# Kernel optimization log

Hardware: AMD Instinct MI355X
Metric: run time of the kernel (lower is better)

Reference implementation:

```python
import jax, jax.numpy as jnp
import numpy as np
import math

H = 128  # hidden_dim
RADIUS = 30.0


def _lin(x, w, b):
    return x @ w + b


def _masked_softmax(logits, mask):
    return jax.nn.softmax(jnp.where(mask, logits, -1e9), axis=-1)


def setup_inputs() -> dict:
    key = jax.random.key(0)
    ks = iter(jax.random.split(key, 64))

    def p(shape, s=0.02):
        return (jax.random.normal(next(ks), shape, jnp.float32) * s)

    B, N, T, M, L = 2, 48, 24, 192, 20
    inp = {
        'agents_state': jax.random.normal(next(ks), (B, N, T, 5), jnp.float32),
        'agents_mask': jnp.ones((B, N, T), jnp.float32),
        'map_polylines': jax.random.normal(next(ks), (B, M, L, 2), jnp.float32),
        'map_poly_mask': jnp.ones((B, M), jnp.float32),
        'map_poly_type': jax.random.randint(next(ks), (B, M), 0, 4),
        'map_tl_status': jax.random.randint(next(ks), (B, M), 0, 8),
        'map_on_route': jax.random.randint(next(ks), (B, M), 0, 2),
        # AgentStateEncoder
        'ae_w0': p((5, H)), 'ae_b0': p((H,)), 'ae_w1': p((H, H)), 'ae_b1': p((H,)),
        'ae_w2': p((H, H)), 'ae_b2': p((H,)),
        # MapPolylineNodeEncoder point_mlp
        'mp_w0': p((2, H)), 'mp_b0': p((H,)), 'mp_w1': p((H, H)), 'mp_b1': p((H,)),
        'type_emb': p((4, H)), 'tl_emb': p((8, H)), 'route_emb': p((2, H)),
        'mo_w0': p((H, H)), 'mo_b0': p((H,)), 'mo_w1': p((H, H)), 'mo_b1': p((H,)),
        # map_rel_mlp (3 -> H -> 1)
        'mr_w0': p((3, H)), 'mr_b0': p((H,)), 'mr_w1': p((H, 1)), 'mr_b1': p((1,)),
        # nbr_rel_mlp (5 -> H -> 1)
        'nr_w0': p((5, H)), 'nr_b0': p((H,)), 'nr_w1': p((H, 1)), 'nr_b1': p((1,)),
        # tau_out (3H -> H -> 64)
        'to_w0': p((3 * H, H)), 'to_b0': p((H,)), 'to_w1': p((H, 64)), 'to_b1': p((64,)),
    }
    return inp


def reference(agents_state, agents_mask, map_polylines, map_poly_mask,
              map_poly_type, map_tl_status, map_on_route,
              ae_w0, ae_b0, ae_w1, ae_b1, ae_w2, ae_b2,
              mp_w0, mp_b0, mp_w1, mp_b1, type_emb, tl_emb, route_emb,
              mo_w0, mo_b0, mo_w1, mo_b1,
              mr_w0, mr_b0, mr_w1, mr_b1,
              nr_w0, nr_b0, nr_w1, nr_b1,
              to_w0, to_b0, to_w1, to_b1):
    B, N, T, _ = agents_state.shape
    a_mask = agents_mask > 0.5
    a_feat = agents_state[..., :5]

    # --- MapPolylineNodeEncoder ---
    m = map_poly_mask > 0.5
    h = jax.nn.relu(_lin(jax.nn.relu(_lin(map_polylines, mp_w0, mp_b0)), mp_w1, mp_b1))  # B,M,L,H
    h = h.max(axis=2)  # B,M,H
    pt = jnp.clip(map_poly_type, 0, type_emb.shape[0] - 1)
    tl = jnp.clip(map_tl_status, 0, tl_emb.shape[0] - 1)
    rt = jnp.clip(map_on_route, 0, route_emb.shape[0] - 1)
    h = h + type_emb[pt] + tl_emb[tl] + route_emb[rt]
    h = _lin(jax.nn.relu(_lin(h, mo_w0, mo_b0)), mo_w1, mo_b1)
    map_node = h * m[..., None].astype(h.dtype)  # B,M,D
    map_center = map_polylines.mean(axis=2)  # B,M,2

    # --- AgentStateEncoder ---
    a = jax.nn.relu(_lin(a_feat, ae_w0, ae_b0))
    a = jax.nn.relu(_lin(a, ae_w1, ae_b1))
    a_emb = _lin(a, ae_w2, ae_b2) * a_mask[..., None].astype(a.dtype)  # B,N,T,D

    # --- map cross-attention with relative-position bias ---
    agent_pos = a_feat[..., 0:2]
    rel = map_center[:, None, None, :, :] - agent_pos[:, :, :, None, :]  # B,N,T,M,2
    dist = jnp.linalg.norm(rel, axis=-1, keepdims=True)
    rel_feat = jnp.concatenate([rel, dist], axis=-1)  # B,N,T,M,3
    rel_score = _lin(jax.nn.relu(_lin(rel_feat, mr_w0, mr_b0)), mr_w1, mr_b1)[..., 0]  # B,N,T,M
    dot = jnp.einsum('bntd,bmd->bntm', a_emb, map_node) / math.sqrt(map_node.shape[-1])
    attn = _masked_softmax(dot + rel_score, m[:, None, None, :])
    map_ctx = jnp.einsum('bntm,bmd->bntd', attn, map_node)

    # --- neighbor graph attention ---
    pos = a_feat[..., 0:2]
    vel = a_feat[..., 3:5]
    rel_pos = jnp.transpose(pos[:, :, None] - pos[:, None, :], (0, 1, 3, 2, 4))  # B,N,T,N,2
    rel_vel = jnp.transpose(vel[:, :, None] - vel[:, None, :], (0, 1, 3, 2, 4))
    dist_ij = jnp.linalg.norm(rel_pos, axis=-1, keepdims=True)  # B,N,T,N,1
    rel_ij = jnp.concatenate([rel_pos, rel_vel, dist_ij], axis=-1)  # B,N,T,N,5
    nbr_score = _lin(jax.nn.relu(_lin(rel_ij, nr_w0, nr_b0)), nr_w1, nr_b1)[..., 0]  # B,N,T,N

    valid_i = a_mask[..., None]  # B,N,T,1
    valid_j = jnp.transpose(a_mask, (0, 2, 1))[:, None, :, :]  # B,1,T,N
    radius_ok = dist_ij[..., 0] <= RADIUS
    not_self = ~jnp.eye(N, dtype=bool)[None, :, None, :]  # 1,N,1,N
    nbr_mask = valid_i & valid_j & radius_ok & not_self

    dot_n = jnp.einsum('bntd,bjtd->bntj', a_emb, a_emb) / math.sqrt(a_emb.shape[-1])
    w_n = _masked_softmax(dot_n + nbr_score, nbr_mask)  # B,N,T,N
    nbr_ctx = jnp.einsum('bntj,bjtd->bntd', w_n, a_emb)

    tau = jnp.concatenate([a_emb, map_ctx, nbr_ctx], axis=-1)
    tau = _lin(jax.nn.relu(_lin(tau, to_w0, to_b0)), to_w1, to_b1)
    tau = tau * a_mask[..., None].astype(tau.dtype)
    return tau, map_ctx, nbr_ctx
```

## Files before the change

### kernel.cpp

```cpp
#include <hip/hip_runtime.h>
#include <math.h>

#define HH 128
#define BB 2
#define NN 48
#define TT 24
#define MM 192
#define LL 20
#define NT (BB*NN*TT)
#define RSQRT_H 0.08838834764831845f
#define RADIUS_C 30.0f

__global__ __launch_bounds__(512) void k_map_enc(
    const float* __restrict__ polylines, const float* __restrict__ poly_mask,
    const int* __restrict__ ptype, const int* __restrict__ tlst, const int* __restrict__ route,
    const float* __restrict__ mp_w0, const float* __restrict__ mp_b0,
    const float* __restrict__ mp_w1, const float* __restrict__ mp_b1,
    const float* __restrict__ type_emb, const float* __restrict__ tl_emb,
    const float* __restrict__ route_emb,
    const float* __restrict__ mo_w0, const float* __restrict__ mo_b0,
    const float* __restrict__ mo_w1, const float* __restrict__ mo_b1,
    float* __restrict__ map_node, float* __restrict__ map_nodeT,
    float* __restrict__ map_center)
{
    int bm  = blockIdx.x;
    int tid = threadIdx.x;
    int pp  = tid >> 7;
    int c   = tid & 127;

    __shared__ float pts[LL*2];
    __shared__ float h1[LL][HH];
    __shared__ float mx[4][HH];
    __shared__ float hb[HH];
    __shared__ float pr[4][HH];
    __shared__ float hb2[HH];

    if (tid < LL*2) pts[tid] = polylines[(size_t)bm*LL*2 + tid];
    __syncthreads();

    {
        float w0x = mp_w0[c], w0y = mp_w0[HH + c], b0 = mp_b0[c];
        #pragma unroll
        for (int i = 0; i < 5; ++i) {
            int p = pp + 4*i;
            h1[p][c] = fmaxf(fmaf(pts[2*p], w0x, fmaf(pts[2*p+1], w0y, b0)), 0.f);
        }
    }
    if (tid < 2) {
        float s = 0.f;
        for (int p = 0; p < LL; ++p) s += pts[2*p + tid];
        map_center[bm*2 + tid] = s * (1.0f / LL);
    }
    __syncthreads();

    {
        float acc[5];
        float b1 = mp_b1[c];
        #pragma unroll
        for (int i = 0; i < 5; ++i) acc[i] = b1;
        for (int k = 0; k < HH; ++k) {
            float wv = mp_w1[k*HH + c];
            #pragma unroll
            for (int i = 0; i < 5; ++i) acc[i] = fmaf(h1[pp + 4*i][k], wv, acc[i]);
        }
        float m5 = acc[0];
        #pragma unroll
        for (int i = 1; i < 5; ++i) m5 = fmaxf(m5, acc[i]);
        mx[pp][c] = m5;
    }
    __syncthreads();

    if (tid < HH) {
        float hm = fmaxf(fmaxf(mx[0][c], mx[1][c]), fmaxf(mx[2][c], mx[3][c]));
        hm = fmaxf(hm, 0.f);
        int pt = ptype[bm]; pt = pt < 0 ? 0 : (pt > 3 ? 3 : pt);
        int tv = tlst[bm];  tv = tv < 0 ? 0 : (tv > 7 ? 7 : tv);
        int rv = route[bm]; rv = rv < 0 ? 0 : (rv > 1 ? 1 : rv);
        hm += type_emb[pt*HH + c] + tl_emb[tv*HH + c] + route_emb[rv*HH + c];
        hb[c] = hm;
    }
    __syncthreads();

    {
        float s = 0.f;
        int k0 = pp*32;
        for (int k = k0; k < k0 + 32; ++k) s = fmaf(hb[k], mo_w0[k*HH + c], s);
        pr[pp][c] = s;
    }
    __syncthreads();
    if (tid < HH) hb2[c] = fmaxf(pr[0][c] + pr[1][c] + pr[2][c] + pr[3][c] + mo_b0[c], 0.f);
    __syncthreads();
    {
        float s = 0.f;
        int k0 = pp*32;
        for (int k = k0; k < k0 + 32; ++k) s = fmaf(hb2[k], mo_w1[k*HH + c], s);
        pr[pp][c] = s;
    }
    __syncthreads();
    if (tid < HH) {
        float a3 = pr[0][c] + pr[1][c] + pr[2][c] + pr[3][c] + mo_b1[0*HH + c];
        float mk = (poly_mask[bm] > 0.5f) ? 1.f : 0.f;
        float v = a3 * mk;
        map_node[(size_t)bm*HH + c] = v;
        int b = bm / MM, m = bm % MM;
        map_nodeT[((size_t)b*HH + c)*MM + m] = v;
    }
}

__global__ __launch_bounds__(256) void k_agent_enc(
    const float* __restrict__ astate, const float* __restrict__ amask,
    const float* __restrict__ ae_w0, const float* __restrict__ ae_b0,
    const float* __restrict__ ae_w1, const float* __restrict__ ae_b1,
    const float* __restrict__ ae_w2, const float* __restrict__ ae_b2,
    float* __restrict__ a_emb)
{
    int r0  = blockIdx.x * 4;
    int tid = threadIdx.x;
    int h   = tid >> 7;
    int c   = tid & 127;

    __shared__ float xin[4][5];
    __shared__ float h1[4][HH];
    __shared__ float h2[4][HH];
    __shared__ float p1[2][4][HH];

    if (tid < 20) xin[tid/5][tid%5] = astate[(size_t)r0*5 + tid];
    __syncthreads();

    if (h == 0) {
        float b = ae_b0[c];
        float w[5];
        #pragma unroll
        for (int i = 0; i < 5; ++i) w[i] = ae_w0[i*HH + c];
        #pragma unroll
        for (int r = 0; r < 4; ++r) {
            float v = b;
            #pragma unroll
            for (int i = 0; i < 5; ++i) v = fmaf(xin[r][i], w[i], v);
            h1[r][c] = fmaxf(v, 0.f);
        }
    }
    __syncthreads();

    {
        float acc[4] = {0.f, 0.f, 0.f, 0.f};
        int k0 = h*64;
        for (int k = k0; k < k0 + 64; ++k) {
            float wv = ae_w1[k*HH + c];
            #pragma unroll
            for (int r = 0; r < 4; ++r) acc[r] = fmaf(h1[r][k], wv, acc[r]);
        }
        #pragma unroll
        for (int r = 0; r < 4; ++r) p1[h][r][c] = acc[r];
    }
    __syncthreads();
    {
        #pragma unroll
        for (int rr = 0; rr < 2; ++rr) {
            int r = h*2 + rr;
            h2[r][c] = fmaxf(p1[0][r][c] + p1[1][r][c] + ae_b1[c], 0.f);
        }
    }
    __syncthreads();

    {
        float acc[4] = {0.f, 0.f, 0.f, 0.f};
        int k0 = h*64;
        for (int k = k0; k < k0 + 64; ++k) {
            float wv = ae_w2[k*HH + c];
            #pragma unroll
            for (int r = 0; r < 4; ++r) acc[r] = fmaf(h2[r][k], wv, acc[r]);
        }
        #pragma unroll
        for (int r = 0; r < 4; ++r) p1[h][r][c] = acc[r];
    }
    __syncthreads();
    {
        #pragma unroll
        for (int rr = 0; rr < 2; ++rr) {
            int r = h*2 + rr;
            int row = r0 + r;
            float v = (p1[0][r][c] + p1[1][r][c] + ae_b2[c]) * amask[row];
            a_emb[(size_t)row*HH + c] = v;
        }
    }
}

__global__ __launch_bounds__(256) void k_map_attn(
    const float* __restrict__ astate,
    const float* __restrict__ a_emb, const float* __restrict__ map_node,
    const float* __restrict__ map_nodeT, const float* __restrict__ map_center,
    const float* __restrict__ poly_mask,
    const float* __restrict__ mr_w0, const float* __restrict__ mr_b0,
    const float* __restrict__ mr_w1, const float* __restrict__ mr_b1,
    float* __restrict__ map_ctx)
{
    int bnt0 = blockIdx.x * 4;
    int b    = bnt0 / (NN*TT);
    int tid  = threadIdx.x;

    __shared__ float  mnL[16][MM];
    __shared__ float4 w4L[HH];
    __shared__ float  w1L[HH];
    __shared__ float4 aq4L[HH];
    __shared__ float  lg[4][MM];
    __shared__ float4 p4L[MM];
    __shared__ float  invL[4];
    __shared__ float  pc[2][4][HH];

    if (tid < HH) {
        int k = tid;
        w4L[k] = make_float4(mr_w0[k], mr_w0[HH+k], mr_w0[2*HH+k], mr_b0[k]);
        w1L[k] = mr_w1[k];
    }
    for (int idx = tid; idx < 4*HH; idx += 256) {
        int r = idx >> 7, k = idx & 127;
        ((float*)&aq4L[k])[r] = a_emb[(size_t)(bnt0 + r)*HH + k];
    }

    float rx[4], ry[4], rd[4];
    if (tid < MM) {
        float mcx = map_center[(b*MM + tid)*2];
        float mcy = map_center[(b*MM + tid)*2 + 1];
        #pragma unroll
        for (int r = 0; r < 4; ++r) {
            float px = astate[(size_t)(bnt0 + r)*5];
            float py = astate[(size_t)(bnt0 + r)*5 + 1];
            rx[r] = mcx - px; ry[r] = mcy - py;
            rd[r] = sqrtf(rx[r]*rx[r] + ry[r]*ry[r]);
        }
    }

    const float* mnT = map_nodeT + (size_t)b*HH*MM;
    float4 st[3];
    #pragma unroll
    for (int i = 0; i < 3; ++i) {
        int q = tid + 256*i;
        int kk = q / 48, mq = q % 48;
        st[i] = *(const float4*)(mnT + (size_t)kk*MM + mq*4);
    }
    float s[4]  = {0.f,0.f,0.f,0.f};
    float dt[4] = {0.f,0.f,0.f,0.f};
    for (int ch = 0; ch < 8; ++ch) {
        __syncthreads();
        #pragma unroll
        for (int i = 0; i < 3; ++i) {
            int q = tid + 256*i;
            int kk = q / 48, mq = q % 48;
            *(float4*)&mnL[kk][mq*4] = st[i];
        }
        __syncthreads();
        if (ch < 7) {
            #pragma unroll
            for (int i = 0; i < 3; ++i) {
                int q = tid + 256*i;
                int kk = q / 48, mq = q % 48;
                st[i] = *(const float4*)(mnT + (size_t)(ch+1)*16*MM + (size_t)kk*MM + mq*4);
            }
        }
        if (tid < MM) {
            int k0 = ch*16;
            #pragma unroll
            for (int kk = 0; kk < 16; ++kk) {
                int k = k0 + kk;
                float4 w  = w4L[k];
                float  w1 = w1L[k];
                float4 aq = aq4L[k];
                float  mn = mnL[kk][tid];
                #pragma unroll
                for (int r = 0; r < 4; ++r) {
                    float hv = fmaf(rx[r], w.x, fmaf(ry[r], w.y, fmaf(rd[r], w.z, w.w)));
                    s[r] = fmaf(fmaxf(hv, 0.f), w1, s[r]);
                }
                dt[0] = fmaf(aq.x, mn, dt[0]);
                dt[1] = fmaf(aq.y, mn, dt[1]);
                dt[2] = fmaf(aq.z, mn, dt[2]);
                dt[3] = fmaf(aq.w, mn, dt[3]);
            }
        }
    }

    if (tid < MM) {
        float pm = poly_mask[b*MM + tid];
        float b1 = mr_b1[0];
        #pragma unroll
        for (int r = 0; r < 4; ++r) {
            float lgt = fmaf(dt[r], RSQRT_H, s[r] + b1);
            lg[r][tid] = (pm > 0.5f) ? lgt : -1e9f;
        }
    }
    __syncthreads();

    {
        int r = tid >> 6, l = tid & 63;
        float v = fmaxf(fmaxf(lg[r][l], lg[r][l+64]), lg[r][l+128]);
        #pragma unroll
        for (int o = 32; o > 0; o >>= 1) v = fmaxf(v, __shfl_xor(v, o));
        float e0 = expf(lg[r][l] - v);
        float e1 = expf(lg[r][l+64] - v);
        float e2 = expf(lg[r][l+128] - v);
        lg[r][l] = e0; lg[r][l+64] = e1; lg[r][l+128] = e2;
        float sm = e0 + e1 + e2;
        #pragma unroll
        for (int o = 32; o > 0; o >>= 1) sm += __shfl_xor(sm, o);
        if (l == 0) invL[r] = 1.0f / sm;
    }
    __syncthreads();
    if (tid < MM) {
        p4L[tid] = make_float4(lg[0][tid]*invL[0], lg[1][tid]*invL[1],
                               lg[2][tid]*invL[2], lg[3][tid]*invL[3]);
    }
    __syncthreads();

    {
        int half = tid >> 7, c = tid & 127;
        float a0=0.f, a1=0.f, a2=0.f, a3=0.f;
        const float* mnb = map_node + ((size_t)b*MM + half*96)*HH + c;
        for (int m = 0; m < 96; ++m) {
            float mv = mnb[(size_t)m*HH];
            float4 p = p4L[half*96 + m];
            a0 = fmaf(p.x, mv, a0); a1 = fmaf(p.y, mv, a1);
            a2 = fmaf(p.z, mv, a2); a3 = fmaf(p.w, mv, a3);
        }
        pc[half][0][c]=a0; pc[half][1][c]=a1; pc[half][2][c]=a2; pc[half][3][c]=a3;
    }
    __syncthreads();
    for (int idx = tid; idx < 4*HH; idx += 256) {
        int r = idx >> 7, c = idx & 127;
        map_ctx[(size_t)(bnt0 + r)*HH + c] = pc[0][r][c] + pc[1][r][c];
    }
}

__global__ __launch_bounds__(256) void k_nbr_attn(
    const float* __restrict__ astate, const float* __restrict__ amask,
    const float* __restrict__ a_emb,
    const float* __restrict__ nr_w0, const float* __restrict__ nr_b0,
    const float* __restrict__ nr_w1, const float* __restrict__ nr_b1,
    float* __restrict__ nbr_ctx)
{
    int bid = blockIdx.x;
    int b   = bid / (TT*8);
    int rem = bid % (TT*8);
    int t   = rem / 8;
    int n0  = (rem % 8) * 6;
    int tid = threadIdx.x;

    __shared__ float  aVL[NN][129];
    __shared__ float  pjL[NN][8];
    __shared__ float4 wAL[HH], wBL[HH];
    __shared__ float  aqL[HH][8];
    __shared__ float  sPL[4][6][NN], dPL[4][6][NN];
    __shared__ float  lgL[6][NN];
    __shared__ float  pL[NN][8];
    __shared__ float  pcL[2][6][HH];

    if (tid < NN) {
        int rj = (b*NN + tid)*TT + t;
        pjL[tid][0] = astate[(size_t)rj*5];
        pjL[tid][1] = astate[(size_t)rj*5 + 1];
        pjL[tid][2] = astate[(size_t)rj*5 + 3];
        pjL[tid][3] = astate[(size_t)rj*5 + 4];
        pjL[tid][4] = amask[rj];
    }
    if (tid < HH) {
        int k = tid;
        wAL[k] = make_float4(nr_w0[k], nr_w0[HH+k], nr_w0[2*HH+k], nr_w0[3*HH+k]);
        wBL[k] = make_float4(nr_w0[4*HH+k], nr_b0[k], nr_w1[k], 0.f);
    }
    #pragma unroll
    for (int i = 0; i < 6; ++i) {
        int q = tid + 256*i;
        int j = q >> 5, cq = q & 31;
        float4 v = *(const float4*)(a_emb + ((size_t)(b*NN + j)*TT + t)*HH + cq*4);
        aVL[j][cq*4+0] = v.x; aVL[j][cq*4+1] = v.y;
        aVL[j][cq*4+2] = v.z; aVL[j][cq*4+3] = v.w;
    }
    __syncthreads();
    for (int idx = tid; idx < 6*HH; idx += 256) {
        int r = idx >> 7, k = idx & 127;
        aqL[k][r] = aVL[n0 + r][k];
    }
    __syncthreads();

    int j  = tid % 48;
    int kg = tid / 48;
    float s[6]  = {0,0,0,0,0,0};
    float dt[6] = {0,0,0,0,0,0};
    if (kg < 4) {
        float jx = pjL[j][0], jy = pjL[j][1], jvx = pjL[j][2], jvy = pjL[j][3];
        float dx[6], dy[6], dvx[6], dvy[6], dd[6];
        #pragma unroll
        for (int r = 0; r < 6; ++r) {
            dx[r]  = pjL[n0+r][0] - jx;  dy[r]  = pjL[n0+r][1] - jy;
            dvx[r] = pjL[n0+r][2] - jvx; dvy[r] = pjL[n0+r][3] - jvy;
            dd[r]  = sqrtf(dx[r]*dx[r] + dy[r]*dy[r]);
        }
        int k0 = kg*32;
        for (int kk = 0; kk < 32; ++kk) {
            int k = k0 + kk;
            float4 wa = wAL[k], wb = wBL[k];
            float4 aA = *(const float4*)&aqL[k][0];
            float4 aB = *(const float4*)&aqL[k][4];
            float  av = aVL[j][k];
            #pragma unroll
            for (int r = 0; r < 6; ++r) {
                float hv = fmaf(dx[r], wa.x, fmaf(dy[r], wa.y,
                           fmaf(dvx[r], wa.z, fmaf(dvy[r], wa.w,
                           fmaf(dd[r], wb.x, wb.y)))));
                s[r] = fmaf(fmaxf(hv, 0.f), wb.z, s[r]);
            }
            dt[0] = fmaf(aA.x, av, dt[0]); dt[1] = fmaf(aA.y, av, dt[1]);
            dt[2] = fmaf(aA.z, av, dt[2]); dt[3] = fmaf(aA.w, av, dt[3]);
            dt[4] = fmaf(aB.x, av, dt[4]); dt[5] = fmaf(aB.y, av, dt[5]);
        }
        #pragma unroll
        for (int r = 0; r < 6; ++r) { sPL[kg][r][j] = s[r]; dPL[kg][r][j] = dt[r]; }
    }
    __syncthreads();

    float b1 = nr_b1[0];
    for (int idx = tid; idx < 6*NN; idx += 256) {
        int r = idx / NN, jj = idx % NN;
        int ni = n0 + r;
        float ss = sPL[0][r][jj] + sPL[1][r][jj] + sPL[2][r][jj] + sPL[3][r][jj] + b1;
        float do2 = dPL[0][r][jj] + dPL[1][r][jj] + dPL[2][r][jj] + dPL[3][r][jj];
        float ddx = pjL[ni][0] - pjL[jj][0];
        float ddy = pjL[ni][1] - pjL[jj][1];
        float dist = sqrtf(ddx*ddx + ddy*ddy);
        bool ok = (pjL[ni][4] > 0.5f) && (pjL[jj][4] > 0.5f) &&
                  (dist <= RADIUS_C) && (jj != ni);
        lgL[r][jj] = ok ? fmaf(do2, RSQRT_H, ss) : -1e9f;
    }
    __syncthreads();

    {
        int wv = tid >> 6, l = tid & 63;
        for (int r = wv; r < 6; r += 4) {
            float v = (l < NN) ? lgL[r][l] : -3.4e38f;
            #pragma unroll
            for (int o = 32; o > 0; o >>= 1) v = fmaxf(v, __shfl_xor(v, o));
            float e = (l < NN) ? expf(lgL[r][l] - v) : 0.f;
            float sm = e;
            #pragma unroll
            for (int o = 32; o > 0; o >>= 1) sm += __shfl_xor(sm, o);
            if (l < NN) lgL[r][l] = e / sm;
        }
    }
    __syncthreads();
    if (tid < NN) {
        #pragma unroll
        for (int r = 0; r < 6; ++r) pL[tid][r] = lgL[r][tid];
        pL[tid][6] = 0.f; pL[tid][7] = 0.f;
    }
    __syncthreads();

    {
        int half = tid >> 7, c = tid & 127;
        float acc[6] = {0,0,0,0,0,0};
        for (int jj = half*24; jj < half*24 + 24; ++jj) {
            float av = aVL[jj][c];
            float4 pA = *(const float4*)&pL[jj][0];
            float4 pB = *(const float4*)&pL[jj][4];
            acc[0] = fmaf(pA.x, av, acc[0]); acc[1] = fmaf(pA.y, av, acc[1]);
            acc[2] = fmaf(pA.z, av, acc[2]); acc[3] = fmaf(pA.w, av, acc[3]);
            acc[4] = fmaf(pB.x, av, acc[4]); acc[5] = fmaf(pB.y, av, acc[5]);
        }
        #pragma unroll
        for (int r = 0; r < 6; ++r) pcL[half][r][c] = acc[r];
    }
    __syncthreads();
    for (int idx = tid; idx < 6*HH; idx += 256) {
        int r = idx >> 7, c = idx & 127;
        int row = (b*NN + n0 + r)*TT + t;
        nbr_ctx[(size_t)row*HH + c] = pcL[0][r][c] + pcL[1][r][c];
    }
}

__global__ __launch_bounds__(512) void k_tau(
    const float* __restrict__ amask,
    const float* __restrict__ a_emb, const float* __restrict__ map_ctx,
    const float* __restrict__ nbr_ctx,
    const float* __restrict__ to_w0, const float* __restrict__ to_b0,
    const float* __restrict__ to_w1, const float* __restrict__ to_b1,
    float* __restrict__ tau)
{
    int r0  = blockIdx.x * 8;
    int tid = threadIdx.x;
    __shared__ float xinT[3*HH][8];
    __shared__ float p1L[4][8][HH];
    __shared__ float h1T[HH][8];
    __shared__ float p2L[8][8][64];

    #pragma unroll
    for (int i = 0; i < 2; ++i) {
        int q = tid + 512*i;
        if (q < 768) {
            int r = q / 96, kq = q % 96;
            const float* src;
            int co;
            if (kq < 32)      { src = a_emb;   co = kq; }
            else if (kq < 64) { src = map_ctx; co = kq - 32; }
            else              { src = nbr_ctx; co = kq - 64; }
            float4 v = *(const float4*)(src + (size_t)(r0 + r)*HH + co*4);
            int kbase = (kq < 32 ? 0 : (kq < 64 ? HH : 2*HH)) + co*4;
            xinT[kbase+0][r] = v.x; xinT[kbase+1][r] = v.y;
            xinT[kbase+2][r] = v.z; xinT[kbase+3][r] = v.w;
        }
    }
    __syncthreads();
    {
        int c = tid & 127, h = tid >> 7;
        float acc[8] = {0,0,0,0,0,0,0,0};
        for (int k = h*96; k < h*96 + 96; ++k) {
            float wv = to_w0[k*HH + c];
            float4 xa = *(const float4*)&xinT[k][0];
            float4 xb = *(const float4*)&xinT[k][4];
            acc[0]=fmaf(xa.x,wv,acc[0]); acc[1]=fmaf(xa.y,wv,acc[1]);
            acc[2]=fmaf(xa.z,wv,acc[2]); acc[3]=fmaf(xa.w,wv,acc[3]);
            acc[4]=fmaf(xb.x,wv,acc[4]); acc[5]=fmaf(xb.y,wv,acc[5]);
            acc[6]=fmaf(xb.z,wv,acc[6]); acc[7]=fmaf(xb.w,wv,acc[7]);
        }
        #pragma unroll
        for (int r = 0; r < 8; ++r) p1L[h][r][c] = acc[r];
    }
    __syncthreads();
    for (int idx = tid; idx < 8*HH; idx += 512) {
        int r = idx >> 7, k = idx & 127;
        float v = p1L[0][r][k] + p1L[1][r][k] + p1L[2][r][k] + p1L[3][r][k] + to_b0[k];
        h1T[k][r] = fmaxf(v, 0.f);
    }
    __syncthreads();
    {
        int c2 = tid & 63, h2 = tid >> 6;
        float acc[8] = {0,0,0,0,0,0,0,0};
        for (int k = h2*16; k < h2*16 + 16; ++k) {
            float wv = to_w1[k*64 + c2];
            float4 xa = *(const float4*)&h1T[k][0];
            float4 xb = *(const float4*)&h1T[k][4];
            acc[0]=fmaf(xa.x,wv,acc[0]); acc[1]=fmaf(xa.y,wv,acc[1]);
            acc[2]=fmaf(xa.z,wv,acc[2]); acc[3]=fmaf(xa.w,wv,acc[3]);
            acc[4]=fmaf(xb.x,wv,acc[4]); acc[5]=fmaf(xb.y,wv,acc[5]);
            acc[6]=fmaf(xb.z,wv,acc[6]); acc[7]=fmaf(xb.w,wv,acc[7]);
        }
        #pragma unroll
        for (int r = 0; r < 8; ++r) p2L[h2][r][c2] = acc[r];
    }
    __syncthreads();
    {
        int r = tid >> 6, c2 = tid & 63;
        float v = 0.f;
        #pragma unroll
        for (int h2 = 0; h2 < 8; ++h2) v += p2L[h2][r][c2];
        v = (v + to_b1[c2]) * amask[r0 + r];
        tau[(size_t)(r0 + r)*64 + c2] = v;
    }
}

extern "C" void kernel_launch(void* const* d_in, const int* in_sizes, int n_in,
                              void* d_out, int out_size, void* d_ws, size_t ws_size,
                              hipStream_t stream)
{
    const float* astate    = (const float*)d_in[0];
    const float* amask     = (const float*)d_in[1];
    const float* polylines = (const float*)d_in[2];
    const float* poly_mask = (const float*)d_in[3];
    const int*   ptype     = (const int*)d_in[4];
    const int*   tlst      = (const int*)d_in[5];
    const int*   route     = (const int*)d_in[6];
    const float* ae_w0 = (const float*)d_in[7];
    const float* ae_b0 = (const float*)d_in[8];
    const float* ae_w1 = (const float*)d_in[9];
    const float* ae_b1 = (const float*)d_in[10];
    const float* ae_w2 = (const float*)d_in[11];
    const float* ae_b2 = (const float*)d_in[12];
    const float* mp_w0 = (const float*)d_in[13];
    const float* mp_b0 = (const float*)d_in[14];
    const float* mp_w1 = (const float*)d_in[15];
    const float* mp_b1 = (const float*)d_in[16];
    const float* type_emb  = (const float*)d_in[17];
    const float* tl_emb    = (const float*)d_in[18];
    const float* route_emb = (const float*)d_in[19];
    const float* mo_w0 = (const float*)d_in[20];
    const float* mo_b0 = (const float*)d_in[21];
    const float* mo_w1 = (const float*)d_in[22];
    const float* mo_b1 = (const float*)d_in[23];
    const float* mr_w0 = (const float*)d_in[24];
    const float* mr_b0 = (const float*)d_in[25];
    const float* mr_w1 = (const float*)d_in[26];
    const float* mr_b1 = (const float*)d_in[27];
    const float* nr_w0 = (const float*)d_in[28];
    const float* nr_b0 = (const float*)d_in[29];
    const float* nr_w1 = (const float*)d_in[30];
    const float* nr_b1 = (const float*)d_in[31];
    const float* to_w0 = (const float*)d_in[32];
    const float* to_b0 = (const float*)d_in[33];
    const float* to_w1 = (const float*)d_in[34];
    const float* to_b1 = (const float*)d_in[35];

    float* tau     = (float*)d_out;
    float* map_ctx = (float*)d_out + (size_t)NT*64;
    float* nbr_ctx = map_ctx + (size_t)NT*HH;

    float* ws         = (float*)d_ws;
    float* a_emb      = ws;
    float* map_node   = a_emb + (size_t)NT*HH;
    float* map_nodeT  = map_node + (size_t)BB*MM*HH;
    float* map_center = map_nodeT + (size_t)BB*MM*HH;

    k_map_enc<<<BB*MM, 512, 0, stream>>>(polylines, poly_mask, ptype, tlst, route,
        mp_w0, mp_b0, mp_w1, mp_b1, type_emb, tl_emb, route_emb,
        mo_w0, mo_b0, mo_w1, mo_b1, map_node, map_nodeT, map_center);

    k_agent_enc<<<NT/4, 256, 0, stream>>>(astate, amask,
        ae_w0, ae_b0, ae_w1, ae_b1, ae_w2, ae_b2, a_emb);

    k_map_attn<<<NT/4, 256, 0, stream>>>(astate, a_emb, map_node, map_nodeT,
        map_center, poly_mask, mr_w0, mr_b0, mr_w1, mr_b1, map_ctx);

    k_nbr_attn<<<BB*TT*8, 256, 0, stream>>>(astate, amask, a_emb,
        nr_w0, nr_b0, nr_w1, nr_b1, nbr_ctx);

    k_tau<<<NT/8, 512, 0, stream>>>(amask, a_emb, map_ctx, nbr_ctx,
        to_w0, to_b0, to_w1, to_b1, tau);
}
```

Measured before the change: 202.7 us.

## Fuse all stages into one persistent kernel with grid barriers

Replaces the five separate kernel launches with a single persistent kernel of 512 blocks that loops over tasks and uses atomic-counter grid barriers between the encoder, attention and output stages. Shared memory is a union of per-stage structs, and each stage is reworked to run with 256 threads (map encoder and tau now use 2-way instead of 4/8-way k splits). The aim is to remove launch overhead and tail gaps between the small stages. In exchange it needs all 512 blocks co-resident for the spin barrier to avoid deadlock, adds a memset, and gives less parallelism per task in some stages.

```diff
diff --git a/kernel.cpp b/kernel.cpp
--- a/kernel.cpp
+++ b/kernel.cpp
@@ -10,169 +10,167 @@
 #define NT (BB*NN*TT)
 #define RSQRT_H 0.08838834764831845f
 #define RADIUS_C 30.0f
-
-__global__ __launch_bounds__(512) void k_map_enc(
-    const float* __restrict__ polylines, const float* __restrict__ poly_mask,
-    const int* __restrict__ ptype, const int* __restrict__ tlst, const int* __restrict__ route,
-    const float* __restrict__ mp_w0, const float* __restrict__ mp_b0,
-    const float* __restrict__ mp_w1, const float* __restrict__ mp_b1,
-    const float* __restrict__ type_emb, const float* __restrict__ tl_emb,
-    const float* __restrict__ route_emb,
-    const float* __restrict__ mo_w0, const float* __restrict__ mo_b0,
-    const float* __restrict__ mo_w1, const float* __restrict__ mo_b1,
-    float* __restrict__ map_node, float* __restrict__ map_nodeT,
-    float* __restrict__ map_center)
-{
-    int bm  = blockIdx.x;
-    int tid = threadIdx.x;
-    int pp  = tid >> 7;
-    int c   = tid & 127;
-
-    __shared__ float pts[LL*2];
-    __shared__ float h1[LL][HH];
-    __shared__ float mx[4][HH];
-    __shared__ float hb[HH];
-    __shared__ float pr[4][HH];
-    __shared__ float hb2[HH];
-
-    if (tid < LL*2) pts[tid] = polylines[(size_t)bm*LL*2 + tid];
-    __syncthreads();
-
-    {
-        float w0x = mp_w0[c], w0y = mp_w0[HH + c], b0 = mp_b0[c];
-        #pragma unroll
-        for (int i = 0; i < 5; ++i) {
-            int p = pp + 4*i;
-            h1[p][c] = fmaxf(fmaf(pts[2*p], w0x, fmaf(pts[2*p+1], w0y, b0)), 0.f);
+#define NBLK 512
+
+struct P {
+    const float *astate, *amask, *polylines, *poly_mask;
+    const int *ptype, *tlst, *route;
+    const float *ae_w0,*ae_b0,*ae_w1,*ae_b1,*ae_w2,*ae_b2;
+    const float *mp_w0,*mp_b0,*mp_w1,*mp_b1;
+    const float *type_emb,*tl_emb,*route_emb;
+    const float *mo_w0,*mo_b0,*mo_w1,*mo_b1;
+    const float *mr_w0,*mr_b0,*mr_w1,*mr_b1;
+    const float *nr_w0,*nr_b0,*nr_w1,*nr_b1;
+    const float *to_w0,*to_b0,*to_w1,*to_b1;
+    float *tau,*map_ctx,*nbr_ctx;
+    float *a_emb,*map_node,*map_nodeT,*map_center;
+    unsigned *bar;
+};
+
+struct SME { float pts[LL*2]; float h1[LL][HH]; float mx[2][HH]; float hb[HH]; float pr[2][HH]; float hb2[HH]; };
+struct SAG { float xin[4][5]; float h1[4][HH]; float h2[4][HH]; float p1[2][4][HH]; };
+struct SMA { float mnL[16][MM]; float w4L[HH][4]; float w1L[HH]; float aq4L[HH][4]; float lg[4][MM]; float p4L[MM][4]; float invL[4]; float pc[2][4][HH]; };
+struct SNB { float aVL[NN][129]; float pjL[NN][8]; float wAL[HH][4]; float wBL[HH][4]; float aqL[HH][8]; float sPL[4][6][NN]; float dPL[4][6][NN]; float lgL[6][NN]; float pL[NN][8]; float pcL[2][6][HH]; };
+struct STA { float xinT[3*HH][4]; float p1L[2][4][HH]; float h1T[HH][4]; };
+
+__device__ __forceinline__ void grid_barrier(unsigned* bar, int which, unsigned nb) {
+    __syncthreads();
+    if (threadIdx.x == 0) {
+        __threadfence();
+        unsigned* cnt = bar + which*32;
+        unsigned* flg = bar + which*32 + 16;
+        unsigned v = __hip_atomic_fetch_add(cnt, 1u, __ATOMIC_ACQ_REL, __HIP_MEMORY_SCOPE_AGENT);
+        if (v == nb - 1u) {
+            __hip_atomic_store(flg, 1u, __ATOMIC_RELEASE, __HIP_MEMORY_SCOPE_AGENT);
+        } else {
+            while (__hip_atomic_load(flg, __ATOMIC_ACQUIRE, __HIP_MEMORY_SCOPE_AGENT) == 0u) {
+                __builtin_amdgcn_s_sleep(8);
+            }
+        }
+        __threadfence();
+    }
+    __syncthreads();
+}
+
+__device__ void do_map_enc(const P& p, SME& s, int bm) {
+    int tid = threadIdx.x, pp = tid >> 7, c = tid & 127;
+    __syncthreads();
+    if (tid < LL*2) s.pts[tid] = p.polylines[(size_t)bm*LL*2 + tid];
+    __syncthreads();
+    {
+        float w0x = p.mp_w0[c], w0y = p.mp_w0[HH + c], b0 = p.mp_b0[c];
+        #pragma unroll
+        for (int i = 0; i < 10; ++i) {
+            int pt_ = pp + 2*i;
+            s.h1[pt_][c] = fmaxf(fmaf(s.pts[2*pt_], w0x, fmaf(s.pts[2*pt_+1], w0y, b0)), 0.f);
         }
     }
     if (tid < 2) {
-        float s = 0.f;
-        for (int p = 0; p < LL; ++p) s += pts[2*p + tid];
-        map_center[bm*2 + tid] = s * (1.0f / LL);
-    }
-    __syncthreads();
-
-    {
-        float acc[5];
-        float b1 = mp_b1[c];
-        #pragma unroll
-        for (int i = 0; i < 5; ++i) acc[i] = b1;
+        float sum = 0.f;
+        for (int q = 0; q < LL; ++q) sum += s.pts[2*q + tid];
+        p.map_center[bm*2 + tid] = sum * (1.0f / LL);
+    }
+    __syncthreads();
+    {
+        float acc[10];
+        float b1 = p.mp_b1[c];
+        #pragma unroll
+        for (int i = 0; i < 10; ++i) acc[i] = b1;
         for (int k = 0; k < HH; ++k) {
-            float wv = mp_w1[k*HH + c];
-            #pragma unroll
-            for (int i = 0; i < 5; ++i) acc[i] = fmaf(h1[pp + 4*i][k], wv, acc[i]);
-        }
-        float m5 = acc[0];
-        #pragma unroll
-        for (int i = 1; i < 5; ++i) m5 = fmaxf(m5, acc[i]);
-        mx[pp][c] = m5;
-    }
-    __syncthreads();
-
+            float wv = p.mp_w1[k*HH + c];
+            #pragma unroll
+            for (int i = 0; i < 10; ++i) acc[i] = fmaf(s.h1[pp + 2*i][k], wv, acc[i]);
+        }
+        float m10 = acc[0];
+        #pragma unroll
+        for (int i = 1; i < 10; ++i) m10 = fmaxf(m10, acc[i]);
+        s.mx[pp][c] = m10;
+    }
+    __syncthreads();
     if (tid < HH) {
-        float hm = fmaxf(fmaxf(mx[0][c], mx[1][c]), fmaxf(mx[2][c], mx[3][c]));
-        hm = fmaxf(hm, 0.f);
-        int pt = ptype[bm]; pt = pt < 0 ? 0 : (pt > 3 ? 3 : pt);
-        int tv = tlst[bm];  tv = tv < 0 ? 0 : (tv > 7 ? 7 : tv);
-        int rv = route[bm]; rv = rv < 0 ? 0 : (rv > 1 ? 1 : rv);
-        hm += type_emb[pt*HH + c] + tl_emb[tv*HH + c] + route_emb[rv*HH + c];
-        hb[c] = hm;
-    }
-    __syncthreads();
-
-    {
-        float s = 0.f;
-        int k0 = pp*32;
-        for (int k = k0; k < k0 + 32; ++k) s = fmaf(hb[k], mo_w0[k*HH + c], s);
-        pr[pp][c] = s;
-    }
-    __syncthreads();
-    if (tid < HH) hb2[c] = fmaxf(pr[0][c] + pr[1][c] + pr[2][c] + pr[3][c] + mo_b0[c], 0.f);
-    __syncthreads();
-    {
-        float s = 0.f;
-        int k0 = pp*32;
-        for (int k = k0; k < k0 + 32; ++k) s = fmaf(hb2[k], mo_w1[k*HH + c], s);
-        pr[pp][c] = s;
+        float hm = fmaxf(fmaxf(s.mx[0][c], s.mx[1][c]), 0.f);
+        int pt = p.ptype[bm]; pt = pt < 0 ? 0 : (pt > 3 ? 3 : pt);
+        int tv = p.tlst[bm];  tv = tv < 0 ? 0 : (tv > 7 ? 7 : tv);
+        int rv = p.route[bm]; rv = rv < 0 ? 0 : (rv > 1 ? 1 : rv);
+        hm += p.type_emb[pt*HH + c] + p.tl_emb[tv*HH + c] + p.route_emb[rv*HH + c];
+        s.hb[c] = hm;
+    }
+    __syncthreads();
+    {
+        float sum = 0.f;
+        int k0 = pp*64;
+        for (int k = k0; k < k0 + 64; ++k) sum = fmaf(s.hb[k], p.mo_w0[k*HH + c], sum);
+        s.pr[pp][c] = sum;
+    }
+    __syncthreads();
+    if (tid < HH) s.hb2[c] = fmaxf(s.pr[0][c] + s.pr[1][c] + p.mo_b0[c], 0.f);
+    __syncthreads();
+    {
+        float sum = 0.f;
+        int k0 = pp*64;
+        for (int k = k0; k < k0 + 64; ++k) sum = fmaf(s.hb2[k], p.mo_w1[k*HH + c], sum);
+        s.pr[pp][c] = sum;
     }
     __syncthreads();
     if (tid < HH) {
-        float a3 = pr[0][c] + pr[1][c] + pr[2][c] + pr[3][c] + mo_b1[0*HH + c];
-        float mk = (poly_mask[bm] > 0.5f) ? 1.f : 0.f;
+        float a3 = s.pr[0][c] + s.pr[1][c] + p.mo_b1[c];
+        float mk = (p.poly_mask[bm] > 0.5f) ? 1.f : 0.f;
         float v = a3 * mk;
-        map_node[(size_t)bm*HH + c] = v;
+        p.map_node[(size_t)bm*HH + c] = v;
         int b = bm / MM, m = bm % MM;
-        map_nodeT[((size_t)b*HH + c)*MM + m] = v;
-    }
-}
-
-__global__ __launch_bounds__(256) void k_agent_enc(
-    const float* __restrict__ astate, const float* __restrict__ amask,
-    const float* __restrict__ ae_w0, const float* __restrict__ ae_b0,
-    const float* __restrict__ ae_w1, const float* __restrict__ ae_b1,
-    const float* __restrict__ ae_w2, const float* __restrict__ ae_b2,
-    float* __restrict__ a_emb)
-{
-    int r0  = blockIdx.x * 4;
-    int tid = threadIdx.x;
-    int h   = tid >> 7;
-    int c   = tid & 127;
-
-    __shared__ float xin[4][5];
-    __shared__ float h1[4][HH];
-    __shared__ float h2[4][HH];
-    __shared__ float p1[2][4][HH];
-
-    if (tid < 20) xin[tid/5][tid%5] = astate[(size_t)r0*5 + tid];
-    __syncthreads();
-
+        p.map_nodeT[((size_t)b*HH + c)*MM + m] = v;
+    }
+}
+
+__device__ void do_agent_enc(const P& p, SAG& s, int r0) {
+    int tid = threadIdx.x, h = tid >> 7, c = tid & 127;
+    __syncthreads();
+    if (tid < 20) s.xin[tid/5][tid%5] = p.astate[(size_t)r0*5 + tid];
+    __syncthreads();
     if (h == 0) {
-        float b = ae_b0[c];
+        float b = p.ae_b0[c];
         float w[5];
         #pragma unroll
-        for (int i = 0; i < 5; ++i) w[i] = ae_w0[i*HH + c];
+        for (int i = 0; i < 5; ++i) w[i] = p.ae_w0[i*HH + c];
         #pragma unroll
         for (int r = 0; r < 4; ++r) {
             float v = b;
             #pragma unroll
-            for (int i = 0; i < 5; ++i) v = fmaf(xin[r][i], w[i], v);
-            h1[r][c] = fmaxf(v, 0.f);
-        }
-    }
-    __syncthreads();
-
-    {
-        float acc[4] = {0.f, 0.f, 0.f, 0.f};
+            for (int i = 0; i < 5; ++i) v = fmaf(s.xin[r][i], w[i], v);
+            s.h1[r][c] = fmaxf(v, 0.f);
+        }
+    }
+    __syncthreads();
+    {
+        float acc[4] = {0.f,0.f,0.f,0.f};
         int k0 = h*64;
         for (int k = k0; k < k0 + 64; ++k) {
-            float wv = ae_w1[k*HH + c];
-            #pragma unroll
-            for (int r = 0; r < 4; ++r) acc[r] = fmaf(h1[r][k], wv, acc[r]);
-        }
-        #pragma unroll
-        for (int r = 0; r < 4; ++r) p1[h][r][c] = acc[r];
+            float wv = p.ae_w1[k*HH + c];
+            #pragma unroll
+            for (int r = 0; r < 4; ++r) acc[r] = fmaf(s.h1[r][k], wv, acc[r]);
+        }
+        #pragma unroll
+        for (int r = 0; r < 4; ++r) s.p1[h][r][c] = acc[r];
     }
     __syncthreads();
     {
         #pragma unroll
         for (int rr = 0; rr < 2; ++rr) {
             int r = h*2 + rr;
-            h2[r][c] = fmaxf(p1[0][r][c] + p1[1][r][c] + ae_b1[c], 0.f);
-        }
-    }
-    __syncthreads();
-
-    {
-        float acc[4] = {0.f, 0.f, 0.f, 0.f};
+            s.h2[r][c] = fmaxf(s.p1[0][r][c] + s.p1[1][r][c] + p.ae_b1[c], 0.f);
+        }
+    }
+    __syncthreads();
+    {
+        float acc[4] = {0.f,0.f,0.f,0.f};
         int k0 = h*64;
         for (int k = k0; k < k0 + 64; ++k) {
-            float wv = ae_w2[k*HH + c];
-            #pragma unroll
-            for (int r = 0; r < 4; ++r) acc[r] = fmaf(h2[r][k], wv, acc[r]);
-        }
-        #pragma unroll
-        for (int r = 0; r < 4; ++r) p1[h][r][c] = acc[r];
+            float wv = p.ae_w2[k*HH + c];
+            #pragma unroll
+            for (int r = 0; r < 4; ++r) acc[r] = fmaf(s.h2[r][k], wv, acc[r]);
+        }
+        #pragma unroll
+        for (int r = 0; r < 4; ++r) s.p1[h][r][c] = acc[r];
     }
     __syncthreads();
     {
@@ -180,58 +178,41 @@
         for (int rr = 0; rr < 2; ++rr) {
             int r = h*2 + rr;
             int row = r0 + r;
-            float v = (p1[0][r][c] + p1[1][r][c] + ae_b2[c]) * amask[row];
-            a_emb[(size_t)row*HH + c] = v;
-        }
-    }
-}
-
-__global__ __launch_bounds__(256) void k_map_attn(
-    const float* __restrict__ astate,
-    const float* __restrict__ a_emb, const float* __restrict__ map_node,
-    const float* __restrict__ map_nodeT, const float* __restrict__ map_center,
-    const float* __restrict__ poly_mask,
-    const float* __restrict__ mr_w0, const float* __restrict__ mr_b0,
-    const float* __restrict__ mr_w1, const float* __restrict__ mr_b1,
-    float* __restrict__ map_ctx)
-{
-    int bnt0 = blockIdx.x * 4;
-    int b    = bnt0 / (NN*TT);
-    int tid  = threadIdx.x;
-
-    __shared__ float  mnL[16][MM];
-    __shared__ float4 w4L[HH];
-    __shared__ float  w1L[HH];
-    __shared__ float4 aq4L[HH];
-    __shared__ float  lg[4][MM];
-    __shared__ float4 p4L[MM];
-    __shared__ float  invL[4];
-    __shared__ float  pc[2][4][HH];
+            p.a_emb[(size_t)row*HH + c] = (s.p1[0][r][c] + s.p1[1][r][c] + p.ae_b2[c]) * p.amask[row];
+        }
+    }
+}
+
+__device__ void do_map_attn(const P& p, SMA& s, int bnt0) {
+    int b   = bnt0 / (NN*TT);
+    int tid = threadIdx.x;
+    __syncthreads();
 
     if (tid < HH) {
         int k = tid;
-        w4L[k] = make_float4(mr_w0[k], mr_w0[HH+k], mr_w0[2*HH+k], mr_b0[k]);
-        w1L[k] = mr_w1[k];
+        s.w4L[k][0] = p.mr_w0[k];      s.w4L[k][1] = p.mr_w0[HH+k];
+        s.w4L[k][2] = p.mr_w0[2*HH+k]; s.w4L[k][3] = p.mr_b0[k];
+        s.w1L[k]    = p.mr_w1[k];
     }
     for (int idx = tid; idx < 4*HH; idx += 256) {
         int r = idx >> 7, k = idx & 127;
-        ((float*)&aq4L[k])[r] = a_emb[(size_t)(bnt0 + r)*HH + k];
+        s.aq4L[k][r] = p.a_emb[(size_t)(bnt0 + r)*HH + k];
     }
 
     float rx[4], ry[4], rd[4];
     if (tid < MM) {
-        float mcx = map_center[(b*MM + tid)*2];
-        float mcy = map_center[(b*MM + tid)*2 + 1];
+        float mcx = p.map_center[(b*MM + tid)*2];
+        float mcy = p.map_center[(b*MM + tid)*2 + 1];
         #pragma unroll
         for (int r = 0; r < 4; ++r) {
-            float px = astate[(size_t)(bnt0 + r)*5];
-            float py = astate[(size_t)(bnt0 + r)*5 + 1];
+            float px = p.astate[(size_t)(bnt0 + r)*5];
+            float py = p.astate[(size_t)(bnt0 + r)*5 + 1];
             rx[r] = mcx - px; ry[r] = mcy - py;
             rd[r] = sqrtf(rx[r]*rx[r] + ry[r]*ry[r]);
         }
     }
 
-    const float* mnT = map_nodeT + (size_t)b*HH*MM;
+    const float* mnT = p.map_nodeT + (size_t)b*HH*MM;
     float4 st[3];
     #pragma unroll
     for (int i = 0; i < 3; ++i) {
@@ -239,15 +220,15 @@
         int kk = q / 48, mq = q % 48;
         st[i] = *(const float4*)(mnT + (size_t)kk*MM + mq*4);
     }
-    float s[4]  = {0.f,0.f,0.f,0.f};
-    float dt[4] = {0.f,0.f,0.f,0.f};
+    float sacc[4] = {0.f,0.f,0.f,0.f};
+    float dt[4]   = {0.f,0.f,0.f,0.f};
     for (int ch = 0; ch < 8; ++ch) {
         __syncthreads();
         #pragma unroll
         for (int i = 0; i < 3; ++i) {
             int q = tid + 256*i;
             int kk = q / 48, mq = q % 48;
-            *(float4*)&mnL[kk][mq*4] = st[i];
+            *(float4*)&s.mnL[kk][mq*4] = st[i];
         }
         __syncthreads();
         if (ch < 7) {
@@ -263,194 +244,185 @@
             #pragma unroll
             for (int kk = 0; kk < 16; ++kk) {
                 int k = k0 + kk;
-                float4 w  = w4L[k];
-                float  w1 = w1L[k];
-                float4 aq = aq4L[k];
-                float  mn = mnL[kk][tid];
+                float wx = s.w4L[k][0], wy = s.w4L[k][1], wz = s.w4L[k][2], wb = s.w4L[k][3];
+                float w1 = s.w1L[k];
+                float mn = s.mnL[kk][tid];
                 #pragma unroll
                 for (int r = 0; r < 4; ++r) {
-                    float hv = fmaf(rx[r], w.x, fmaf(ry[r], w.y, fmaf(rd[r], w.z, w.w)));
-                    s[r] = fmaf(fmaxf(hv, 0.f), w1, s[r]);
+                    float hv = fmaf(rx[r], wx, fmaf(ry[r], wy, fmaf(rd[r], wz, wb)));
+                    sacc[r] = fmaf(fmaxf(hv, 0.f), w1, sacc[r]);
                 }
-                dt[0] = fmaf(aq.x, mn, dt[0]);
-                dt[1] = fmaf(aq.y, mn, dt[1]);
-                dt[2] = fmaf(aq.z, mn, dt[2]);
-                dt[3] = fmaf(aq.w, mn, dt[3]);
+                dt[0] = fmaf(s.aq4L[k][0], mn, dt[0]);
+                dt[1] = fmaf(s.aq4L[k][1], mn, dt[1]);
+                dt[2] = fmaf(s.aq4L[k][2], mn, dt[2]);
+                dt[3] = fmaf(s.aq4L[k][3], mn, dt[3]);
             }
         }
     }
 
     if (tid < MM) {
-        float pm = poly_mask[b*MM + tid];
-        float b1 = mr_b1[0];
+        float pm = p.poly_mask[b*MM + tid];
+        float b1 = p.mr_b1[0];
         #pragma unroll
         for (int r = 0; r < 4; ++r) {
-            float lgt = fmaf(dt[r], RSQRT_H, s[r] + b1);
-            lg[r][tid] = (pm > 0.5f) ? lgt : -1e9f;
+            float lgt = fmaf(dt[r], RSQRT_H, sacc[r] + b1);
+            s.lg[r][tid] = (pm > 0.5f) ? lgt : -1e9f;
         }
     }
     __syncthreads();
 
     {
         int r = tid >> 6, l = tid & 63;
-        float v = fmaxf(fmaxf(lg[r][l], lg[r][l+64]), lg[r][l+128]);
+        float v = fmaxf(fmaxf(s.lg[r][l], s.lg[r][l+64]), s.lg[r][l+128]);
         #pragma unroll
         for (int o = 32; o > 0; o >>= 1) v = fmaxf(v, __shfl_xor(v, o));
-        float e0 = expf(lg[r][l] - v);
-        float e1 = expf(lg[r][l+64] - v);
-        float e2 = expf(lg[r][l+128] - v);
-        lg[r][l] = e0; lg[r][l+64] = e1; lg[r][l+128] = e2;
+        float e0 = expf(s.lg[r][l] - v);
+        float e1 = expf(s.lg[r][l+64] - v);
+        float e2 = expf(s.lg[r][l+128] - v);
+        s.lg[r][l] = e0; s.lg[r][l+64] = e1; s.lg[r][l+128] = e2;
         float sm = e0 + e1 + e2;
         #pragma unroll
         for (int o = 32; o > 0; o >>= 1) sm += __shfl_xor(sm, o);
-        if (l == 0) invL[r] = 1.0f / sm;
+        if (l == 0) s.invL[r] = 1.0f / sm;
     }
     __syncthreads();
     if (tid < MM) {
-        p4L[tid] = make_float4(lg[0][tid]*invL[0], lg[1][tid]*invL[1],
-                               lg[2][tid]*invL[2], lg[3][tid]*invL[3]);
+        s.p4L[tid][0] = s.lg[0][tid]*s.invL[0];
+        s.p4L[tid][1] = s.lg[1][tid]*s.invL[1];
+        s.p4L[tid][2] = s.lg[2][tid]*s.invL[2];
+        s.p4L[tid][3] = s.lg[3][tid]*s.invL[3];
     }
     __syncthreads();
 
     {
         int half = tid >> 7, c = tid & 127;
         float a0=0.f, a1=0.f, a2=0.f, a3=0.f;
-        const float* mnb = map_node + ((size_t)b*MM + half*96)*HH + c;
+        const float* mnb = p.map_node + ((size_t)b*MM + half*96)*HH + c;
         for (int m = 0; m < 96; ++m) {
             float mv = mnb[(size_t)m*HH];
-            float4 p = p4L[half*96 + m];
-            a0 = fmaf(p.x, mv, a0); a1 = fmaf(p.y, mv, a1);
-            a2 = fmaf(p.z, mv, a2); a3 = fmaf(p.w, mv, a3);
-        }
-        pc[half][0][c]=a0; pc[half][1][c]=a1; pc[half][2][c]=a2; pc[half][3][c]=a3;
+            float4 pp4 = *(const float4*)&s.p4L[half*96 + m][0];
+            a0 = fmaf(pp4.x, mv, a0); a1 = fmaf(pp4.y, mv, a1);
+            a2 = fmaf(pp4.z, mv, a2); a3 = fmaf(pp4.w, mv, a3);
+        }
+        s.pc[half][0][c]=a0; s.pc[half][1][c]=a1; s.pc[half][2][c]=a2; s.pc[half][3][c]=a3;
     }
     __syncthreads();
     for (int idx = tid; idx < 4*HH; idx += 256) {
         int r = idx >> 7, c = idx & 127;
-        map_ctx[(size_t)(bnt0 + r)*HH + c] = pc[0][r][c] + pc[1][r][c];
-    }
-}
-
-__global__ __launch_bounds__(256) void k_nbr_attn(
-    const float* __restrict__ astate, const float* __restrict__ amask,
-    const float* __restrict__ a_emb,
-    const float* __restrict__ nr_w0, const float* __restrict__ nr_b0,
-    const float* __restrict__ nr_w1, const float* __restrict__ nr_b1,
-    float* __restrict__ nbr_ctx)
-{
-    int bid = blockIdx.x;
-    int b   = bid / (TT*8);
-    int rem = bid % (TT*8);
+        p.map_ctx[(size_t)(bnt0 + r)*HH + c] = s.pc[0][r][c] + s.pc[1][r][c];
+    }
+}
+
+__device__ void do_nbr_attn(const P& p, SNB& s, int task) {
+    int b   = task / (TT*8);
+    int rem = task % (TT*8);
     int t   = rem / 8;
     int n0  = (rem % 8) * 6;
     int tid = threadIdx.x;
-
-    __shared__ float  aVL[NN][129];
-    __shared__ float  pjL[NN][8];
-    __shared__ float4 wAL[HH], wBL[HH];
-    __shared__ float  aqL[HH][8];
-    __shared__ float  sPL[4][6][NN], dPL[4][6][NN];
-    __shared__ float  lgL[6][NN];
-    __shared__ float  pL[NN][8];
-    __shared__ float  pcL[2][6][HH];
+    __syncthreads();
 
     if (tid < NN) {
         int rj = (b*NN + tid)*TT + t;
-        pjL[tid][0] = astate[(size_t)rj*5];
-        pjL[tid][1] = astate[(size_t)rj*5 + 1];
-        pjL[tid][2] = astate[(size_t)rj*5 + 3];
-        pjL[tid][3] = astate[(size_t)rj*5 + 4];
-        pjL[tid][4] = amask[rj];
+        s.pjL[tid][0] = p.astate[(size_t)rj*5];
+        s.pjL[tid][1] = p.astate[(size_t)rj*5 + 1];
+        s.pjL[tid][2] = p.astate[(size_t)rj*5 + 3];
+        s.pjL[tid][3] = p.astate[(size_t)rj*5 + 4];
+        s.pjL[tid][4] = p.amask[rj];
     }
     if (tid < HH) {
         int k = tid;
-        wAL[k] = make_float4(nr_w0[k], nr_w0[HH+k], nr_w0[2*HH+k], nr_w0[3*HH+k]);
-        wBL[k] = make_float4(nr_w0[4*HH+k], nr_b0[k], nr_w1[k], 0.f);
+        s.wAL[k][0] = p.nr_w0[k];      s.wAL[k][1] = p.nr_w0[HH+k];
+        s.wAL[k][2] = p.nr_w0[2*HH+k]; s.wAL[k][3] = p.nr_w0[3*HH+k];
+        s.wBL[k][0] = p.nr_w0[4*HH+k]; s.wBL[k][1] = p.nr_b0[k];
+        s.wBL[k][2] = p.nr_w1[k];      s.wBL[k][3] = 0.f;
     }
     #pragma unroll
     for (int i = 0; i < 6; ++i) {
         int q = tid + 256*i;
         int j = q >> 5, cq = q & 31;
-        float4 v = *(const float4*)(a_emb + ((size_t)(b*NN + j)*TT + t)*HH + cq*4);
-        aVL[j][cq*4+0] = v.x; aVL[j][cq*4+1] = v.y;
-        aVL[j][cq*4+2] = v.z; aVL[j][cq*4+3] = v.w;
+        float4 v = *(const float4*)(p.a_emb + ((size_t)(b*NN + j)*TT + t)*HH + cq*4);
+        s.aVL[j][cq*4+0] = v.x; s.aVL[j][cq*4+1] = v.y;
+        s.aVL[j][cq*4+2] = v.z; s.aVL[j][cq*4+3] = v.w;
     }
     __syncthreads();
     for (int idx = tid; idx < 6*HH; idx += 256) {
         int r = idx >> 7, k = idx & 127;
-        aqL[k][r] = aVL[n0 + r][k];
-    }
-    __syncthreads();
-
-    int j  = tid % 48;
-    int kg = tid / 48;
-    float s[6]  = {0,0,0,0,0,0};
-    float dt[6] = {0,0,0,0,0,0};
-    if (kg < 4) {
-        float jx = pjL[j][0], jy = pjL[j][1], jvx = pjL[j][2], jvy = pjL[j][3];
-        float dx[6], dy[6], dvx[6], dvy[6], dd[6];
-        #pragma unroll
-        for (int r = 0; r < 6; ++r) {
-            dx[r]  = pjL[n0+r][0] - jx;  dy[r]  = pjL[n0+r][1] - jy;
-            dvx[r] = pjL[n0+r][2] - jvx; dvy[r] = pjL[n0+r][3] - jvy;
-            dd[r]  = sqrtf(dx[r]*dx[r] + dy[r]*dy[r]);
-        }
-        int k0 = kg*32;
-        for (int kk = 0; kk < 32; ++kk) {
-            int k = k0 + kk;
-            float4 wa = wAL[k], wb = wBL[k];
-            float4 aA = *(const float4*)&aqL[k][0];
-            float4 aB = *(const float4*)&aqL[k][4];
-            float  av = aVL[j][k];
+        s.aqL[k][r] = s.aVL[n0 + r][k];
+    }
+    __syncthreads();
+
+    {
+        int j  = tid % 48;
+        int kg = tid / 48;
+        if (kg < 4) {
+            float jx = s.pjL[j][0], jy = s.pjL[j][1], jvx = s.pjL[j][2], jvy = s.pjL[j][3];
+            float dx[6], dy[6], dvx[6], dvy[6], dd[6];
             #pragma unroll
             for (int r = 0; r < 6; ++r) {
-                float hv = fmaf(dx[r], wa.x, fmaf(dy[r], wa.y,
-                           fmaf(dvx[r], wa.z, fmaf(dvy[r], wa.w,
-                           fmaf(dd[r], wb.x, wb.y)))));
-                s[r] = fmaf(fmaxf(hv, 0.f), wb.z, s[r]);
+                dx[r]  = s.pjL[n0+r][0] - jx;  dy[r]  = s.pjL[n0+r][1] - jy;
+                dvx[r] = s.pjL[n0+r][2] - jvx; dvy[r] = s.pjL[n0+r][3] - jvy;
+                dd[r]  = sqrtf(dx[r]*dx[r] + dy[r]*dy[r]);
             }
-            dt[0] = fmaf(aA.x, av, dt[0]); dt[1] = fmaf(aA.y, av, dt[1]);
-            dt[2] = fmaf(aA.z, av, dt[2]); dt[3] = fmaf(aA.w, av, dt[3]);
-            dt[4] = fmaf(aB.x, av, dt[4]); dt[5] = fmaf(aB.y, av, dt[5]);
-        }
-        #pragma unroll
-        for (int r = 0; r < 6; ++r) { sPL[kg][r][j] = s[r]; dPL[kg][r][j] = dt[r]; }
-    }
-    __syncthreads();
-
-    float b1 = nr_b1[0];
+            float sr[6]  = {0,0,0,0,0,0};
+            float dt[6] = {0,0,0,0,0,0};
+            int k0 = kg*32;
+            for (int kk = 0; kk < 32; ++kk) {
+                int k = k0 + kk;
+                float wax = s.wAL[k][0], way = s.wAL[k][1], waz = s.wAL[k][2], waw = s.wAL[k][3];
+                float wbx = s.wBL[k][0], wby = s.wBL[k][1], wbz = s.wBL[k][2];
+                float4 aA = *(const float4*)&s.aqL[k][0];
+                float4 aB = *(const float4*)&s.aqL[k][4];
+                float  av = s.aVL[j][k];
+                #pragma unroll
+                for (int r = 0; r < 6; ++r) {
+                    float hv = fmaf(dx[r], wax, fmaf(dy[r], way,
+                               fmaf(dvx[r], waz, fmaf(dvy[r], waw,
+                               fmaf(dd[r], wbx, wby)))));
+                    sr[r] = fmaf(fmaxf(hv, 0.f), wbz, sr[r]);
+                }
+                dt[0] = fmaf(aA.x, av, dt[0]); dt[1] = fmaf(aA.y, av, dt[1]);
+                dt[2] = fmaf(aA.z, av, dt[2]); dt[3] = fmaf(aA.w, av, dt[3]);
+                dt[4] = fmaf(aB.x, av, dt[4]); dt[5] = fmaf(aB.y, av, dt[5]);
+            }
+            #pragma unroll
+            for (int r = 0; r < 6; ++r) { s.sPL[kg][r][j] = sr[r]; s.dPL[kg][r][j] = dt[r]; }
+        }
+    }
+    __syncthreads();
+
+    float b1 = p.nr_b1[0];
     for (int idx = tid; idx < 6*NN; idx += 256) {
         int r = idx / NN, jj = idx % NN;
         int ni = n0 + r;
-        float ss = sPL[0][r][jj] + sPL[1][r][jj] + sPL[2][r][jj] + sPL[3][r][jj] + b1;
-        float do2 = dPL[0][r][jj] + dPL[1][r][jj] + dPL[2][r][jj] + dPL[3][r][jj];
-        float ddx = pjL[ni][0] - pjL[jj][0];
-        float ddy = pjL[ni][1] - pjL[jj][1];
+        float ss  = s.sPL[0][r][jj] + s.sPL[1][r][jj] + s.sPL[2][r][jj] + s.sPL[3][r][jj] + b1;
+        float do2 = s.dPL[0][r][jj] + s.dPL[1][r][jj] + s.dPL[2][r][jj] + s.dPL[3][r][jj];
+        float ddx = s.pjL[ni][0] - s.pjL[jj][0];
+        float ddy = s.pjL[ni][1] - s.pjL[jj][1];
         float dist = sqrtf(ddx*ddx + ddy*ddy);
-        bool ok = (pjL[ni][4] > 0.5f) && (pjL[jj][4] > 0.5f) &&
+        bool ok = (s.pjL[ni][4] > 0.5f) && (s.pjL[jj][4] > 0.5f) &&
                   (dist <= RADIUS_C) && (jj != ni);
-        lgL[r][jj] = ok ? fmaf(do2, RSQRT_H, ss) : -1e9f;
+        s.lgL[r][jj] = ok ? fmaf(do2, RSQRT_H, ss) : -1e9f;
     }
     __syncthreads();
 
     {
         int wv = tid >> 6, l = tid & 63;
         for (int r = wv; r < 6; r += 4) {
-            float v = (l < NN) ? lgL[r][l] : -3.4e38f;
+            float v = (l < NN) ? s.lgL[r][l] : -3.4e38f;
             #pragma unroll
             for (int o = 32; o > 0; o >>= 1) v = fmaxf(v, __shfl_xor(v, o));
-            float e = (l < NN) ? expf(lgL[r][l] - v) : 0.f;
+            float e = (l < NN) ? expf(s.lgL[r][l] - v) : 0.f;
             float sm = e;
             #pragma unroll
             for (int o = 32; o > 0; o >>= 1) sm += __shfl_xor(sm, o);
-            if (l < NN) lgL[r][l] = e / sm;
+            if (l < NN) s.lgL[r][l] = e / sm;
         }
     }
     __syncthreads();
     if (tid < NN) {
         #pragma unroll
-        for (int r = 0; r < 6; ++r) pL[tid][r] = lgL[r][tid];
-        pL[tid][6] = 0.f; pL[tid][7] = 0.f;
+        for (int r = 0; r < 6; ++r) s.pL[tid][r] = s.lgL[r][tid];
+        s.pL[tid][6] = 0.f; s.pL[tid][7] = 0.f;
     }
     __syncthreads();
 
@@ -458,168 +430,125 @@
         int half = tid >> 7, c = tid & 127;
         float acc[6] = {0,0,0,0,0,0};
         for (int jj = half*24; jj < half*24 + 24; ++jj) {
-            float av = aVL[jj][c];
-            float4 pA = *(const float4*)&pL[jj][0];
-            float4 pB = *(const float4*)&pL[jj][4];
+            float av = s.aVL[jj][c];
+            float4 pA = *(const float4*)&s.pL[jj][0];
+            float4 pB = *(const float4*)&s.pL[jj][4];
             acc[0] = fmaf(pA.x, av, acc[0]); acc[1] = fmaf(pA.y, av, acc[1]);
             acc[2] = fmaf(pA.z, av, acc[2]); acc[3] = fmaf(pA.w, av, acc[3]);
             acc[4] = fmaf(pB.x, av, acc[4]); acc[5] = fmaf(pB.y, av, acc[5]);
         }
         #pragma unroll
-        for (int r = 0; r < 6; ++r) pcL[half][r][c] = acc[r];
+        for (int r = 0; r < 6; ++r) s.pcL[half][r][c] = acc[r];
     }
     __syncthreads();
     for (int idx = tid; idx < 6*HH; idx += 256) {
         int r = idx >> 7, c = idx & 127;
         int row = (b*NN + n0 + r)*TT + t;
-        nbr_ctx[(size_t)row*HH + c] = pcL[0][r][c] + pcL[1][r][c];
-    }
-}
-
-__global__ __launch_bounds__(512) void k_tau(
-    const float* __restrict__ amask,
-    const float* __restrict__ a_emb, const float* __restrict__ map_ctx,
-    const float* __restrict__ nbr_ctx,
-    const float* __restrict__ to_w0, const float* __restrict__ to_b0,
-    const float* __restrict__ to_w1, const float* __restrict__ to_b1,
-    float* __restrict__ tau)
-{
-    int r0  = blockIdx.x * 8;
+        p.nbr_ctx[(size_t)row*HH + c] = s.pcL[0][r][c] + s.pcL[1][r][c];
+    }
+}
+
+__device__ void do_tau(const P& p, STA& s, int r0) {
     int tid = threadIdx.x;
-    __shared__ float xinT[3*HH][8];
-    __shared__ float p1L[4][8][HH];
-    __shared__ float h1T[HH][8];
-    __shared__ float p2L[8][8][64];
-
-    #pragma unroll
-    for (int i = 0; i < 2; ++i) {
-        int q = tid + 512*i;
-        if (q < 768) {
-            int r = q / 96, kq = q % 96;
-            const float* src;
-            int co;
-            if (kq < 32)      { src = a_emb;   co = kq; }
-            else if (kq < 64) { src = map_ctx; co = kq - 32; }
-            else              { src = nbr_ctx; co = kq - 64; }
-            float4 v = *(const float4*)(src + (size_t)(r0 + r)*HH + co*4);
-            int kbase = (kq < 32 ? 0 : (kq < 64 ? HH : 2*HH)) + co*4;
-            xinT[kbase+0][r] = v.x; xinT[kbase+1][r] = v.y;
-            xinT[kbase+2][r] = v.z; xinT[kbase+3][r] = v.w;
-        }
+    __syncthreads();
+    for (int idx = tid; idx < 384; idx += 256) {
+        int r = idx / 96, kq = idx % 96;
+        const float* src; int co;
+        if (kq < 32)      { src = p.a_emb;   co = kq; }
+        else if (kq < 64) { src = p.map_ctx; co = kq - 32; }
+        else              { src = p.nbr_ctx; co = kq - 64; }
+        float4 v = *(const float4*)(src + (size_t)(r0 + r)*HH + co*4);
+        int kb = (kq < 32 ? 0 : (kq < 64 ? HH : 2*HH)) + co*4;
+        s.xinT[kb+0][r] = v.x; s.xinT[kb+1][r] = v.y;
+        s.xinT[kb+2][r] = v.z; s.xinT[kb+3][r] = v.w;
     }
     __syncthreads();
     {
         int c = tid & 127, h = tid >> 7;
-        float acc[8] = {0,0,0,0,0,0,0,0};
-        for (int k = h*96; k < h*96 + 96; ++k) {
-            float wv = to_w0[k*HH + c];
-            float4 xa = *(const float4*)&xinT[k][0];
-            float4 xb = *(const float4*)&xinT[k][4];
+        float acc[4] = {0,0,0,0};
+        for (int k = h*192; k < h*192 + 192; ++k) {
+            float wv = p.to_w0[k*HH + c];
+            float4 xa = *(const float4*)&s.xinT[k][0];
             acc[0]=fmaf(xa.x,wv,acc[0]); acc[1]=fmaf(xa.y,wv,acc[1]);
             acc[2]=fmaf(xa.z,wv,acc[2]); acc[3]=fmaf(xa.w,wv,acc[3]);
-            acc[4]=fmaf(xb.x,wv,acc[4]); acc[5]=fmaf(xb.y,wv,acc[5]);
-            acc[6]=fmaf(xb.z,wv,acc[6]); acc[7]=fmaf(xb.w,wv,acc[7]);
-        }
-        #pragma unroll
-        for (int r = 0; r < 8; ++r) p1L[h][r][c] = acc[r];
-    }
-    __syncthreads();
-    for (int idx = tid; idx < 8*HH; idx += 512) {
+        }
+        #pragma unroll
+        for (int r = 0; r < 4; ++r) s.p1L[h][r][c] = acc[r];
+    }
+    __syncthreads();
+    for (int idx = tid; idx < 4*HH; idx += 256) {
         int r = idx >> 7, k = idx & 127;
-        float v = p1L[0][r][k] + p1L[1][r][k] + p1L[2][r][k] + p1L[3][r][k] + to_b0[k];
-        h1T[k][r] = fmaxf(v, 0.f);
-    }
-    __syncthreads();
-    {
-        int c2 = tid & 63, h2 = tid >> 6;
-        float acc[8] = {0,0,0,0,0,0,0,0};
-        for (int k = h2*16; k < h2*16 + 16; ++k) {
-            float wv = to_w1[k*64 + c2];
-            float4 xa = *(const float4*)&h1T[k][0];
-            float4 xb = *(const float4*)&h1T[k][4];
-            acc[0]=fmaf(xa.x,wv,acc[0]); acc[1]=fmaf(xa.y,wv,acc[1]);
-            acc[2]=fmaf(xa.z,wv,acc[2]); acc[3]=fmaf(xa.w,wv,acc[3]);
-            acc[4]=fmaf(xb.x,wv,acc[4]); acc[5]=fmaf(xb.y,wv,acc[5]);
-            acc[6]=fmaf(xb.z,wv,acc[6]); acc[7]=fmaf(xb.w,wv,acc[7]);
-        }
-        #pragma unroll
-        for (int r = 0; r < 8; ++r) p2L[h2][r][c2] = acc[r];
+        s.h1T[k][r] = fmaxf(s.p1L[0][r][k] + s.p1L[1][r][k] + p.to_b0[k], 0.f);
     }
     __syncthreads();
     {
         int r = tid >> 6, c2 = tid & 63;
-        float v = 0.f;
-        #pragma unroll
-        for (int h2 = 0; h2 < 8; ++h2) v += p2L[h2][r][c2];
-        v = (v + to_b1[c2]) * amask[r0 + r];
-        tau[(size_t)(r0 + r)*64 + c2] = v;
-    }
+        float acc = p.to_b1[c2];
+        for (int k = 0; k < HH; ++k)
+            acc = fmaf(s.h1T[k][r], p.to_w1[k*64 + c2], acc);
+        p.tau[(size_t)(r0 + r)*64 + c2] = acc * p.amask[r0 + r];
+    }
+}
+
+__global__ __launch_bounds__(256, 2) void k_fused(P p) {
+    __shared__ __align__(16) char smraw[sizeof(SNB)];
+
+    for (int task = blockIdx.x; task < 960; task += NBLK) {
+        if (task < 384) do_map_enc(p, *(SME*)smraw, task);
+        else            do_agent_enc(p, *(SAG*)smraw, (task - 384)*4);
+    }
+    grid_barrier(p.bar, 0, NBLK);
+
+    for (int task = blockIdx.x; task < 960; task += NBLK) {
+        if (task < 576) do_map_attn(p, *(SMA*)smraw, task*4);
+        else            do_nbr_attn(p, *(SNB*)smraw, task - 576);
+    }
+    grid_barrier(p.bar, 1, NBLK);
+
+    for (int task = blockIdx.x; task < 576; task += NBLK)
+        do_tau(p, *(STA*)smraw, task*4);
 }
 
 extern "C" void kernel_launch(void* const* d_in, const int* in_sizes, int n_in,
                               void* d_out, int out_size, void* d_ws, size_t ws_size,
                               hipStream_t stream)
 {
-    const float* astate    = (const float*)d_in[0];
-    const float* amask     = (const float*)d_in[1];
-    const float* polylines = (const float*)d_in[2];
-    const float* poly_mask = (const float*)d_in[3];
-    const int*   ptype     = (const int*)d_in[4];
-    const int*   tlst      = (const int*)d_in[5];
-    const int*   route     = (const int*)d_in[6];
-    const float* ae_w0 = (const float*)d_in[7];
-    const float* ae_b0 = (const float*)d_in[8];
-    const float* ae_w1 = (const float*)d_in[9];
-    const float* ae_b1 = (const float*)d_in[10];
-    const float* ae_w2 = (const float*)d_in[11];
-    const float* ae_b2 = (const float*)d_in[12];
-    const float* mp_w0 = (const float*)d_in[13];
-    const float* mp_b0 = (const float*)d_in[14];
-    const float* mp_w1 = (const float*)d_in[15];
-    const float* mp_b1 = (const float*)d_in[16];
-    const float* type_emb  = (const float*)d_in[17];
-    const float* tl_emb    = (const float*)d_in[18];
-    const float* route_emb = (const float*)d_in[19];
-    const float* mo_w0 = (const float*)d_in[20];
-    const float* mo_b0 = (const float*)d_in[21];
-    const float* mo_w1 = (const float*)d_in[22];
-    const float* mo_b1 = (const float*)d_in[23];
-    const float* mr_w0 = (const float*)d_in[24];
-    const float* mr_b0 = (const float*)d_in[25];
-    const float* mr_w1 = (const float*)d_in[26];
-    const float* mr_b1 = (const float*)d_in[27];
-    const float* nr_w0 = (const float*)d_in[28];
-    const float* nr_b0 = (const float*)d_in[29];
-    const float* nr_w1 = (const float*)d_in[30];
-    const float* nr_b1 = (const float*)d_in[31];
-    const float* to_w0 = (const float*)d_in[32];
-    const float* to_b0 = (const float*)d_in[33];
-    const float* to_w1 = (const float*)d_in[34];
-    const float* to_b1 = (const float*)d_in[35];
-
-    float* tau     = (float*)d_out;
-    float* map_ctx = (float*)d_out + (size_t)NT*64;
-    float* nbr_ctx = map_ctx + (size_t)NT*HH;
-
-    float* ws         = (float*)d_ws;
-    float* a_emb      = ws;
-    float* map_node   = a_emb + (size_t)NT*HH;
-    float* map_nodeT  = map_node + (size_t)BB*MM*HH;
-    float* map_center = map_nodeT + (size_t)BB*MM*HH;
-
-    k_map_enc<<<BB*MM, 512, 0, stream>>>(polylines, poly_mask, ptype, tlst, route,
-        mp_w0, mp_b0, mp_w1, mp_b1, type_emb, tl_emb, route_emb,
-        mo_w0, mo_b0, mo_w1, mo_b1, map_node, map_nodeT, map_center);
-
-    k_agent_enc<<<NT/4, 256, 0, stream>>>(astate, amask,
-        ae_w0, ae_b0, ae_w1, ae_b1, ae_w2, ae_b2, a_emb);
-
-    k_map_attn<<<NT/4, 256, 0, stream>>>(astate, a_emb, map_node, map_nodeT,
-        map_center, poly_mask, mr_w0, mr_b0, mr_w1, mr_b1, map_ctx);
-
-    k_nbr_attn<<<BB*TT*8, 256, 0, stream>>>(astate, amask, a_emb,
-        nr_w0, nr_b0, nr_w1, nr_b1, nbr_ctx);
-
-    k_tau<<<NT/8, 512, 0, stream>>>(amask, a_emb, map_ctx, nbr_ctx,
-        to_w0, to_b0, to_w1, to_b1, tau);
-}
+    P p;
+    p.astate    = (const float*)d_in[0];
+    p.amask     = (const float*)d_in[1];
+    p.polylines = (const float*)d_in[2];
+    p.poly_mask = (const float*)d_in[3];
+    p.ptype     = (const int*)d_in[4];
+    p.tlst      = (const int*)d_in[5];
+    p.route     = (const int*)d_in[6];
+    p.ae_w0 = (const float*)d_in[7];  p.ae_b0 = (const float*)d_in[8];
+    p.ae_w1 = (const float*)d_in[9];  p.ae_b1 = (const float*)d_in[10];
+    p.ae_w2 = (const float*)d_in[11]; p.ae_b2 = (const float*)d_in[12];
+    p.mp_w0 = (const float*)d_in[13]; p.mp_b0 = (const float*)d_in[14];
+    p.mp_w1 = (const float*)d_in[15]; p.mp_b1 = (const float*)d_in[16];
+    p.type_emb  = (const float*)d_in[17];
+    p.tl_emb    = (const float*)d_in[18];
+    p.route_emb = (const float*)d_in[19];
+    p.mo_w0 = (const float*)d_in[20]; p.mo_b0 = (const float*)d_in[21];
+    p.mo_w1 = (const float*)d_in[22]; p.mo_b1 = (const float*)d_in[23];
+    p.mr_w0 = (const float*)d_in[24]; p.mr_b0 = (const float*)d_in[25];
+    p.mr_w1 = (const float*)d_in[26]; p.mr_b1 = (const float*)d_in[27];
+    p.nr_w0 = (const float*)d_in[28]; p.nr_b0 = (const float*)d_in[29];
+    p.nr_w1 = (const float*)d_in[30]; p.nr_b1 = (const float*)d_in[31];
+    p.to_w0 = (const float*)d_in[32]; p.to_b0 = (const float*)d_in[33];
+    p.to_w1 = (const float*)d_in[34]; p.to_b1 = (const float*)d_in[35];
+
+    p.tau     = (float*)d_out;
+    p.map_ctx = (float*)d_out + (size_t)NT*64;
+    p.nbr_ctx = p.map_ctx + (size_t)NT*HH;
+
+    p.bar = (unsigned*)d_ws;
+    float* base   = (float*)((char*)d_ws + 256);
+    p.a_emb      = base;
+    p.map_node   = p.a_emb + (size_t)NT*HH;
+    p.map_nodeT  = p.map_node + (size_t)BB*MM*HH;
+    p.map_center = p.map_nodeT + (size_t)BB*MM*HH;
+
+    hipMemsetAsync(d_ws, 0, 256, stream);
+    k_fused<<<NBLK, 256, 0, stream>>>(p);
+}
```

Result: slower. 604.2 us (+198.1%).
